# Performance work log

Hardware: AMD Instinct MI355X
Metric: run time of the kernel (lower is better)

## Reference

```python
import jax, jax.numpy as jnp
import numpy as np

H = 16  # head_count
NEG = -1e18

def setup_inputs() -> dict:
    key = jax.random.key(0)
    ks = jax.random.split(key, 8)
    B, L, D = 4, 2048, 1024
    s = 1.0 / np.sqrt(D)
    return {
        "key":   jax.random.normal(ks[0], (B, L, D), jnp.float32),
        "value": jax.random.normal(ks[1], (B, L, D), jnp.float32),
        "query": jax.random.normal(ks[2], (B, L, D), jnp.float32),
        "mask":  jax.random.randint(ks[3], (B, L, L), 0, 2).astype(bool),
        "Wk": jax.random.normal(ks[4], (D, D), jnp.float32) * s,
        "bk": jnp.zeros((D,), jnp.float32),
        "Wv": jax.random.normal(ks[5], (D, D), jnp.float32) * s,
        "bv": jnp.zeros((D,), jnp.float32),
        "Wq": jax.random.normal(ks[6], (D, D), jnp.float32) * s,
        "bq": jnp.zeros((D,), jnp.float32),
        "Wo": jax.random.normal(ks[7], (D, D), jnp.float32) * s,
        "bo": jnp.zeros((D,), jnp.float32),
    }

def reference(key, value, query, mask, Wk, bk, Wv, bv, Wq, bq, Wo, bo):
    B, Lk, D = key.shape
    Lq = query.shape[1]
    dh = D // H

    def shape(x, L):  # (B, L, D) -> (B, H, L, dh)
        return x.reshape(B, L, H, dh).transpose(0, 2, 1, 3)

    k = shape(key @ Wk + bk, Lk)
    v = shape(value @ Wv + bv, Lk)
    q = shape(query @ Wq + bq, Lq) / jnp.sqrt(jnp.asarray(dh, query.dtype))

    scores = jnp.einsum('bhqd,bhkd->bhqk', q, k).astype(jnp.float32)
    scores = jnp.where(mask[:, None, :, :], NEG, scores)  # masked_fill
    attn = jax.nn.softmax(scores, axis=-1).astype(q.dtype)
    # dropout is identity at inference
    ctx = jnp.einsum('bhqk,bhkd->bhqd', attn, v)
    ctx = ctx.transpose(0, 2, 1, 3).reshape(B, Lq, D)  # unshape
    output = ctx @ Wo + bo
    top_attn = attn[:, 0, :, :]
    return (output, top_attn)
```

## Files before the change

### kernel.cpp

```cpp
#include <hip/hip_runtime.h>
#include <hip/hip_bf16.h>
#include <stdint.h>

#define Bn 4
#define Ln 2048
#define Dn 1024
#define Hn 16
#define DHn 64

typedef __attribute__((ext_vector_type(8))) short short8;
typedef __attribute__((ext_vector_type(4))) float f32x4;
typedef unsigned long long u64;
typedef __hip_bfloat16 bf16;

union U8 { uint32_t u[4]; short8 s; };

__device__ __forceinline__ short f2b(float x) {
  bf16 b = __float2bfloat16(x);
  return *(short*)&b;
}

__device__ __forceinline__ uint32_t cvt_pk_bf16(float lo, float hi) {
  uint32_t r;
  asm("v_cvt_pk_bf16_f32 %0, %1, %2" : "=v"(r) : "v"(lo), "v"(hi));
  return r;
}

__device__ __forceinline__ void gll16(const void* g, void* l) {
  __builtin_amdgcn_global_load_lds(
      (const __attribute__((address_space(1))) void*)g,
      (__attribute__((address_space(3))) void*)l, 16, 0, 0);
}

__global__ __launch_bounds__(256) void f32_to_bf16_3(
    const float* __restrict__ A, const float* __restrict__ B2, const float* __restrict__ C3,
    short* __restrict__ oA, short* __restrict__ oB, short* __restrict__ oC, int n4)
{
  const int z = blockIdx.y;
  const float* in = (z == 0) ? A : (z == 1) ? B2 : C3;
  short* out = (z == 0) ? oA : (z == 1) ? oB : oC;
  int i = blockIdx.x * 256 + threadIdx.x;
  if (i < n4) {
    float4 v = ((const float4*)in)[i];
    short4 o;
    o.x = f2b(v.x); o.y = f2b(v.y); o.z = f2b(v.z); o.w = f2b(v.w);
    ((short4*)out)[i] = o;
  }
}

__global__ __launch_bounds__(256) void transpose_w_bf16(
    const float* __restrict__ W0, const float* __restrict__ W1,
    const float* __restrict__ W2, const float* __restrict__ W3,
    short* __restrict__ WT0, short* __restrict__ WT1,
    short* __restrict__ WT2, short* __restrict__ WT3)
{
  __shared__ float t[64][65];
  const int z = blockIdx.z;
  const float* src = (z == 0) ? W0 : (z == 1) ? W1 : (z == 2) ? W2 : W3;
  short* dst = (z == 0) ? WT0 : (z == 1) ? WT1 : (z == 2) ? WT2 : WT3;
  const int tid = threadIdx.x;
  const int k0 = blockIdx.x * 64, n0 = blockIdx.y * 64;
  #pragma unroll
  for (int it = 0; it < 4; ++it) {
    int idx = it * 256 + tid;
    int row = idx >> 4, c4 = (idx & 15) * 4;
    *(float4*)&t[row][c4] = *(const float4*)&src[(size_t)(k0 + row) * Dn + n0 + c4];
  }
  __syncthreads();
  #pragma unroll
  for (int it = 0; it < 4; ++it) {
    int idx = it * 256 + tid;
    int nr = idx >> 4, kc = (idx & 15) * 4;
    short4 o;
    o.x = f2b(t[kc + 0][nr]); o.y = f2b(t[kc + 1][nr]);
    o.z = f2b(t[kc + 2][nr]); o.w = f2b(t[kc + 3][nr]);
    *(short4*)&dst[(size_t)(n0 + nr) * Dn + k0 + kc] = o;
  }
}

__device__ __forceinline__ void gemm_core(
    const short* __restrict__ Xs, const short* __restrict__ WTs,
    const float* __restrict__ bias, void* __restrict__ Cout,
    int M, int N, int K, float scale, int mode)
{
  __shared__ short lds[2][2 * 128 * 32];
  const int tid  = threadIdx.x;
  const int lane = tid & 63;
  const int wv   = tid >> 6;
  const int quad = lane >> 4;
  const int l16  = lane & 15;
  const int m0 = blockIdx.y * 128, n0 = blockIdx.x * 128;
  const int wm = (wv >> 1) * 64, wn = (wv & 1) * 64;

  f32x4 acc[4][4];
  #pragma unroll
  for (int i = 0; i < 4; ++i)
    #pragma unroll
    for (int j = 0; j < 4; ++j)
      acc[i][j] = (f32x4){0.f, 0.f, 0.f, 0.f};

  #pragma unroll
  for (int r = 0; r < 2; ++r) {
    int idx = r * 256 + tid;
    int row = idx >> 2, kc = idx & 3;
    gll16(Xs  + (size_t)(m0 + row) * K + kc * 8, &lds[0][idx * 8]);
    gll16(WTs + (size_t)(n0 + row) * K + kc * 8, &lds[0][128 * 32 + idx * 8]);
  }
  __syncthreads();

  const int NT = K >> 5;
  int cur = 0;
  for (int t = 0; t < NT; ++t) {
    if (t + 1 < NT) {
      const int kn = (t + 1) * 32;
      #pragma unroll
      for (int r = 0; r < 2; ++r) {
        int idx = r * 256 + tid;
        int row = idx >> 2, kc = idx & 3;
        gll16(Xs  + (size_t)(m0 + row) * K + kn + kc * 8, &lds[cur ^ 1][idx * 8]);
        gll16(WTs + (size_t)(n0 + row) * K + kn + kc * 8, &lds[cur ^ 1][128 * 32 + idx * 8]);
      }
    }
    const short* ldsA = lds[cur];
    const short* ldsB = lds[cur] + 128 * 32;
    short8 af[4], bfr[4];
    #pragma unroll
    for (int i = 0; i < 4; ++i)
      af[i] = *(const short8*)(ldsA + (wm + i * 16 + l16) * 32 + quad * 8);
    #pragma unroll
    for (int j = 0; j < 4; ++j)
      bfr[j] = *(const short8*)(ldsB + (wn + j * 16 + l16) * 32 + quad * 8);
    __builtin_amdgcn_s_setprio(1);
    #pragma unroll
    for (int i = 0; i < 4; ++i)
      #pragma unroll
      for (int j = 0; j < 4; ++j)
        acc[i][j] = __builtin_amdgcn_mfma_f32_16x16x32_bf16(af[i], bfr[j], acc[i][j], 0, 0, 0);
    __builtin_amdgcn_s_setprio(0);
    __syncthreads();
    cur ^= 1;
  }

  if (mode == 0) {
    float* C = (float*)Cout;
    #pragma unroll
    for (int j = 0; j < 4; ++j) {
      int n = n0 + wn + j * 16 + l16;
      float bv = bias[n];
      #pragma unroll
      for (int i = 0; i < 4; ++i) {
        int mb = m0 + wm + i * 16 + quad * 4;
        #pragma unroll
        for (int r = 0; r < 4; ++r)
          C[(size_t)(mb + r) * N + n] = (acc[i][j][r] + bv) * scale;
      }
    }
  } else if (mode == 1) {
    short* C = (short*)Cout;
    #pragma unroll
    for (int j = 0; j < 4; ++j) {
      int n = n0 + wn + j * 16 + l16;
      float bv = bias[n];
      #pragma unroll
      for (int i = 0; i < 4; ++i) {
        int mb = m0 + wm + i * 16 + quad * 4;
        #pragma unroll
        for (int r = 0; r < 4; ++r)
          C[(size_t)(mb + r) * N + n] = f2b((acc[i][j][r] + bv) * scale);
      }
    }
  } else {
    short* C = (short*)Cout;
    #pragma unroll
    for (int j = 0; j < 4; ++j) {
      int n = n0 + wn + j * 16 + l16;
      float bv = bias[n];
      int hh = n >> 6, dd = n & 63;
      #pragma unroll
      for (int i = 0; i < 4; ++i) {
        int mb = m0 + wm + i * 16 + quad * 4;
        int bb = mb >> 11, ll = mb & 2047;
        short4 o;
        o.x = f2b((acc[i][j][0] + bv) * scale);
        o.y = f2b((acc[i][j][1] + bv) * scale);
        o.z = f2b((acc[i][j][2] + bv) * scale);
        o.w = f2b((acc[i][j][3] + bv) * scale);
        *(short4*)&C[((size_t)(bb * 16 + hh) * 64 + dd) * 2048 + ll] = o;
      }
    }
  }
}

__global__ __launch_bounds__(256) void gemm_qkv(
    const short* __restrict__ kc, const short* __restrict__ vc, const short* __restrict__ qc,
    const short* __restrict__ WkT, const short* __restrict__ WvT, const short* __restrict__ WqT,
    const float* __restrict__ bk, const float* __restrict__ bv, const float* __restrict__ bq,
    short* __restrict__ kb, short* __restrict__ vT, short* __restrict__ qb2)
{
  const int z = blockIdx.z;
  const short* Xs = (z == 0) ? kc : (z == 1) ? vc : qc;
  const short* WT = (z == 0) ? WkT : (z == 1) ? WvT : WqT;
  const float* bs = (z == 0) ? bk : (z == 1) ? bv : bq;
  void* C = (z == 0) ? (void*)kb : (z == 1) ? (void*)vT : (void*)qb2;
  float scale = (z == 2) ? 0.125f : 1.0f;
  int mode = (z == 1) ? 2 : 1;
  gemm_core(Xs, WT, bs, C, Bn * Ln, Dn, Dn, scale, mode);
}

__global__ __launch_bounds__(256) void gemm_wo(
    const short* __restrict__ ctx, const short* __restrict__ WoT,
    const float* __restrict__ bo, float* __restrict__ out)
{
  gemm_core(ctx, WoT, bo, out, Bn * Ln, Dn, Dn, 1.0f, 0);
}

__global__ __launch_bounds__(256) void pack_mask(const int* __restrict__ mask, u64* __restrict__ pm)
{
  size_t tg = (size_t)blockIdx.x * 256 + threadIdx.x;
  int v = mask[tg];
  u64 bal = __ballot(v != 0);
  if ((threadIdx.x & 63) == 0) pm[tg >> 6] = bal;
}


__device__ __forceinline__ const short8* ldsfrag(const short* lds, int row, int colb) {
  return (const short8*)((const char*)lds + row * 128 + (colb ^ ((row & 7) << 4)));
}

__global__ __launch_bounds__(256) void attn_fused(
    const short* __restrict__ qb, const short* __restrict__ kb,
    const short* __restrict__ vT, const u64* __restrict__ pm,
    short* __restrict__ ctx_bf, float* __restrict__ topattn,
    float* __restrict__ mtile, float2* __restrict__ stat2)
{
  __shared__ short ldsK[2][64 * 64];
  __shared__ short ldsVT[2][64 * 64];
  const int tid  = threadIdx.x;
  const int lane = tid & 63, wv = tid >> 6;
  const int quad = lane >> 4, l16 = lane & 15;
  const int g = blockIdx.x;
  const int x = (g >> 3) & 31;
  const int c = (g & 7) + ((g >> 8) << 3);
  const int h = c & 15, b = c >> 4;
  const int q0 = x * 64;
  const int q_g = q0 + wv * 16 + l16;

  const short* qrow = qb + (size_t)(b * Ln + q_g) * Dn + h * DHn;
  short8 qf[2];
  qf[0] = *(const short8*)(qrow + quad * 8);
  qf[1] = *(const short8*)(qrow + 32 + quad * 8);

  const u64* pmq = pm + (size_t)(b * Ln + q_g) * 32;
  const short* kbase = kb + (size_t)b * Ln * Dn + h * DHn;
  const short* vbase = vT + (size_t)(b * Hn + h) * DHn * Ln;

  #pragma unroll
  for (int it = 0; it < 2; ++it) {
    int idx = it * 256 + tid;
    int row = idx >> 3, cb = (idx & 7) * 16;
    int scb = cb ^ ((row & 7) << 4);
    gll16(kbase + (size_t)row * Dn + (scb >> 1), &ldsK[0][idx * 8]);
    gll16(vbase + (size_t)row * Ln + (scb >> 1), &ldsVT[0][idx * 8]);
  }
  __syncthreads();

  float m_r = -INFINITY, l_r = 0.f;
  f32x4 oc[4];
  #pragma unroll
  for (int dt = 0; dt < 4; ++dt) oc[dt] = (f32x4){0.f, 0.f, 0.f, 0.f};

  const int srcA = ((lane >> 4) & 1) * 32 + l16;
  const int srcB = srcA + 16;
  const bool hiHalf = (lane & 32) != 0;

  int cur = 0;
  for (int t = 0; t < 32; ++t) {
    const int k0 = t * 64;
    if (t < 31) {
      const int kn = k0 + 64;
      #pragma unroll
      for (int it = 0; it < 2; ++it) {
        int idx = it * 256 + tid;
        int row = idx >> 3, cb = (idx & 7) * 16;
        int scb = cb ^ ((row & 7) << 4);
        gll16(kbase + (size_t)(kn + row) * Dn + (scb >> 1), &ldsK[cur ^ 1][idx * 8]);
        gll16(vbase + (size_t)row * Ln + kn + (scb >> 1), &ldsVT[cur ^ 1][idx * 8]);
      }
    }

    f32x4 sv[4];
    #pragma unroll
    for (int mt = 0; mt < 4; ++mt) sv[mt] = (f32x4){0.f, 0.f, 0.f, 0.f};
    __builtin_amdgcn_s_setprio(1);
    #pragma unroll
    for (int s = 0; s < 2; ++s)
      #pragma unroll
      for (int mt = 0; mt < 4; ++mt) {
        short8 kf = *ldsfrag(&ldsK[cur][0], mt * 16 + l16, s * 64 + quad * 16);
        sv[mt] = __builtin_amdgcn_mfma_f32_16x16x32_bf16(kf, qf[s], sv[mt], 0, 0, 0);
      }
    __builtin_amdgcn_s_setprio(0);

    float tm = fmaxf(fmaxf(sv[0][0], sv[0][1]), fmaxf(sv[0][2], sv[0][3]));
    #pragma unroll
    for (int mt = 1; mt < 4; ++mt)
      tm = fmaxf(tm, fmaxf(fmaxf(sv[mt][0], sv[mt][1]), fmaxf(sv[mt][2], sv[mt][3])));
    tm = fmaxf(tm, __shfl_xor(tm, 16, 64));
    tm = fmaxf(tm, __shfl_xor(tm, 32, 64));
    if (tm > m_r + 8.f) {
      float sc = __expf(m_r - tm);
      l_r *= sc;
      #pragma unroll
      for (int dt = 0; dt < 4; ++dt)
        #pragma unroll
        for (int r = 0; r < 4; ++r) oc[dt][r] *= sc;
      m_r = tm;
    }
    const u64 w = pmq[t];
    float ls = 0.f;
    #pragma unroll
    for (int mt = 0; mt < 4; ++mt) {
      unsigned nib = (unsigned)(w >> (mt * 16 + quad * 4)) & 0xFu;
      #pragma unroll
      for (int r = 0; r < 4; ++r) {
        float p = __expf(sv[mt][r] - m_r);
        p = (nib & (1u << r)) ? 0.f : p;
        sv[mt][r] = p;
        ls += p;
      }
    }
    l_r += ls;

    if (h == 0) {
      float* tpb = topattn + (size_t)(b * Ln + q_g) * Ln + k0 + quad * 4;
      #pragma unroll
      for (int mt = 0; mt < 4; ++mt)
        *(float4*)&tpb[mt * 16] = *(float4*)&sv[mt];
      if (quad == 0) mtile[(size_t)(b * Ln + q_g) * 32 + t] = m_r;
    }

    uint32_t d0[4], d1[4];
    #pragma unroll
    for (int mt = 0; mt < 4; ++mt) {
      d0[mt] = cvt_pk_bf16(sv[mt][0], sv[mt][1]);
      d1[mt] = cvt_pk_bf16(sv[mt][2], sv[mt][3]);
    }

    #pragma unroll
    for (int ks = 0; ks < 2; ++ks) {
      uint32_t a0  = (uint32_t)__shfl((int)d0[2 * ks],     srcA, 64);
      uint32_t a0b = (uint32_t)__shfl((int)d0[2 * ks + 1], srcA, 64);
      uint32_t a1  = (uint32_t)__shfl((int)d1[2 * ks],     srcA, 64);
      uint32_t a1b = (uint32_t)__shfl((int)d1[2 * ks + 1], srcA, 64);
      uint32_t b0  = (uint32_t)__shfl((int)d0[2 * ks],     srcB, 64);
      uint32_t b0b = (uint32_t)__shfl((int)d0[2 * ks + 1], srcB, 64);
      uint32_t b1  = (uint32_t)__shfl((int)d1[2 * ks],     srcB, 64);
      uint32_t b1b = (uint32_t)__shfl((int)d1[2 * ks + 1], srcB, 64);
      U8 u;
      u.u[0] = hiHalf ? a0b : a0;
      u.u[1] = hiHalf ? a1b : a1;
      u.u[2] = hiHalf ? b0b : b0;
      u.u[3] = hiHalf ? b1b : b1;
      short8 pf = u.s;
      __builtin_amdgcn_s_setprio(1);
      #pragma unroll
      for (int dt = 0; dt < 4; ++dt) {
        short8 vf = *ldsfrag(&ldsVT[cur][0], dt * 16 + l16, ks * 64 + quad * 16);
        oc[dt] = __builtin_amdgcn_mfma_f32_16x16x32_bf16(vf, pf, oc[dt], 0, 0, 0);
      }
      __builtin_amdgcn_s_setprio(0);
    }
    __syncthreads();
    cur ^= 1;
  }

  l_r += __shfl_xor(l_r, 16, 64);
  l_r += __shfl_xor(l_r, 32, 64);
  const float rinv = (l_r > 0.f) ? 1.f / l_r : 0.f;

  short* crow = ctx_bf + (size_t)(b * Ln + q_g) * Dn + h * DHn;
  #pragma unroll
  for (int dt = 0; dt < 4; ++dt) {
    short4 o;
    o.x = f2b(oc[dt][0] * rinv); o.y = f2b(oc[dt][1] * rinv);
    o.z = f2b(oc[dt][2] * rinv); o.w = f2b(oc[dt][3] * rinv);
    *(short4*)&crow[dt * 16 + quad * 4] = o;
  }
  if (h == 0 && quad == 0)
    stat2[b * Ln + q_g] = make_float2(m_r, rinv);
}

__global__ __launch_bounds__(256) void topattn_fix(
    float* __restrict__ topattn, const float* __restrict__ mtile,
    const float2* __restrict__ stat2)
{
  const int row = blockIdx.x;
  const float2 st = stat2[row];
  const int tid = threadIdx.x;
  const float sc = __expf(mtile[(size_t)row * 32 + (tid >> 3)] - st.x) * st.y;
  float4* p = (float4*)(topattn + (size_t)row * Ln) + tid * 2;
  float4 a = p[0], b2 = p[1];
  a.x *= sc; a.y *= sc; a.z *= sc; a.w *= sc;
  b2.x *= sc; b2.y *= sc; b2.z *= sc; b2.w *= sc;
  p[0] = a; p[1] = b2;
}

extern "C" void kernel_launch(void* const* d_in, const int* in_sizes, int n_in,
                              void* d_out, int out_size, void* d_ws, size_t ws_size,
                              hipStream_t stream) {
  (void)in_sizes; (void)n_in; (void)out_size; (void)ws_size;
  const float* key   = (const float*)d_in[0];
  const float* value = (const float*)d_in[1];
  const float* query = (const float*)d_in[2];
  const int*   mask  = (const int*)d_in[3];
  const float* Wk = (const float*)d_in[4];
  const float* bk = (const float*)d_in[5];
  const float* Wv = (const float*)d_in[6];
  const float* bv = (const float*)d_in[7];
  const float* Wq = (const float*)d_in[8];
  const float* bq = (const float*)d_in[9];
  const float* Wo = (const float*)d_in[10];
  const float* bo = (const float*)d_in[11];

  char* ws = (char*)d_ws;
  const size_t MiB = 1ull << 20;
  short* kc  = (short*)(ws +   0 * MiB);
  short* vc  = (short*)(ws +  16 * MiB);
  short* qc  = (short*)(ws +  32 * MiB);
  short* WkT = (short*)(ws +  48 * MiB);
  short* WvT = (short*)(ws +  50 * MiB);
  short* WqT = (short*)(ws +  52 * MiB);
  short* WoT = (short*)(ws +  54 * MiB);
  short* qb  = (short*)(ws +  56 * MiB);
  short* kb  = (short*)(ws +  72 * MiB);
  short* vT  = (short*)(ws +  88 * MiB);
  u64*   pm  = (u64*)  (ws + 104 * MiB);
  short* ctx_bf = (short*)(ws + 106 * MiB);
  float* mtile  = (float*)(ws + 122 * MiB);
  float2* stat2 = (float2*)(ws + 123 * MiB);

  float* out     = (float*)d_out;
  float* topattn = out + (size_t)Bn * Ln * Dn;

  const int M = Bn * Ln;
  const int n4 = (M * Dn) / 4;

  f32_to_bf16_3<<<dim3(n4 / 256, 3), 256, 0, stream>>>(key, value, query, kc, vc, qc, n4);
  transpose_w_bf16<<<dim3(16, 16, 4), 256, 0, stream>>>(Wk, Wv, Wq, Wo, WkT, WvT, WqT, WoT);

  gemm_qkv<<<dim3(8, 64, 3), 256, 0, stream>>>(kc, vc, qc, WkT, WvT, WqT, bk, bv, bq, kb, vT, qb);

  pack_mask<<<dim3((Bn * Ln * Ln) / 256), 256, 0, stream>>>(mask, pm);

  attn_fused<<<dim3(2048), 256, 0, stream>>>(qb, kb, vT, pm, ctx_bf, topattn, mtile, stat2);
  topattn_fix<<<dim3(Bn * Ln), 256, 0, stream>>>(topattn, mtile, stat2);

  gemm_wo<<<dim3(8, 64), 256, 0, stream>>>(ctx_bf, WoT, bo, out);
}
```

Measured before the change: 564.7 us.

## Use 128-query tiles with 8 waves and exchange P through LDS

The attention kernel now runs 512 threads per block, with 8 waves covering 128 query rows. Each K/V tile loaded into LDS is therefore shared by twice as many queries, and each thread issues one async load per buffer instead of two. The cross-lane shuffle that rearranged the softmax probabilities into the MFMA B-operand layout is replaced by a write to a per-wave LDS scratch array followed by a vector read. The cost is fewer blocks in the grid, more LDS per block, and extra LDS traffic for P.

```diff
diff --git a/kernel.cpp b/kernel.cpp
--- a/kernel.cpp
+++ b/kernel.cpp
@@ -9,11 +9,10 @@
 #define DHn 64
 
 typedef __attribute__((ext_vector_type(8))) short short8;
+typedef __attribute__((ext_vector_type(4))) short short4v;
 typedef __attribute__((ext_vector_type(4))) float f32x4;
 typedef unsigned long long u64;
 typedef __hip_bfloat16 bf16;
-
-union U8 { uint32_t u[4]; short8 s; };
 
 __device__ __forceinline__ short f2b(float x) {
   bf16 b = __float2bfloat16(x);
@@ -227,7 +226,7 @@
   return (const short8*)((const char*)lds + row * 128 + (colb ^ ((row & 7) << 4)));
 }
 
-__global__ __launch_bounds__(256) void attn_fused(
+__global__ __launch_bounds__(512) void attn_fused(
     const short* __restrict__ qb, const short* __restrict__ kb,
     const short* __restrict__ vT, const u64* __restrict__ pm,
     short* __restrict__ ctx_bf, float* __restrict__ topattn,
@@ -235,14 +234,15 @@
 {
   __shared__ short ldsK[2][64 * 64];
   __shared__ short ldsVT[2][64 * 64];
+  __shared__ short pp[8][16][72];
   const int tid  = threadIdx.x;
   const int lane = tid & 63, wv = tid >> 6;
   const int quad = lane >> 4, l16 = lane & 15;
   const int g = blockIdx.x;
-  const int x = (g >> 3) & 31;
-  const int c = (g & 7) + ((g >> 8) << 3);
+  const int x = (g >> 3) & 15;
+  const int c = ((g >> 7) << 3) | (g & 7);
   const int h = c & 15, b = c >> 4;
-  const int q0 = x * 64;
+  const int q0 = x * 128;
   const int q_g = q0 + wv * 16 + l16;
 
   const short* qrow = qb + (size_t)(b * Ln + q_g) * Dn + h * DHn;
@@ -254,38 +254,24 @@
   const short* kbase = kb + (size_t)b * Ln * Dn + h * DHn;
   const short* vbase = vT + (size_t)(b * Hn + h) * DHn * Ln;
 
-  #pragma unroll
-  for (int it = 0; it < 2; ++it) {
-    int idx = it * 256 + tid;
-    int row = idx >> 3, cb = (idx & 7) * 16;
-    int scb = cb ^ ((row & 7) << 4);
-    gll16(kbase + (size_t)row * Dn + (scb >> 1), &ldsK[0][idx * 8]);
-    gll16(vbase + (size_t)row * Ln + (scb >> 1), &ldsVT[0][idx * 8]);
-  }
+  const int srow = tid >> 3, scb = ((tid & 7) * 16) ^ ((srow & 7) << 4);
+
+  gll16(kbase + (size_t)srow * Dn + (scb >> 1), &ldsK[0][tid * 8]);
+  gll16(vbase + (size_t)srow * Ln + (scb >> 1), &ldsVT[0][tid * 8]);
   __syncthreads();
 
   float m_r = -INFINITY, l_r = 0.f;
   f32x4 oc[4];
   #pragma unroll
   for (int dt = 0; dt < 4; ++dt) oc[dt] = (f32x4){0.f, 0.f, 0.f, 0.f};
-
-  const int srcA = ((lane >> 4) & 1) * 32 + l16;
-  const int srcB = srcA + 16;
-  const bool hiHalf = (lane & 32) != 0;
 
   int cur = 0;
   for (int t = 0; t < 32; ++t) {
     const int k0 = t * 64;
     if (t < 31) {
       const int kn = k0 + 64;
-      #pragma unroll
-      for (int it = 0; it < 2; ++it) {
-        int idx = it * 256 + tid;
-        int row = idx >> 3, cb = (idx & 7) * 16;
-        int scb = cb ^ ((row & 7) << 4);
-        gll16(kbase + (size_t)(kn + row) * Dn + (scb >> 1), &ldsK[cur ^ 1][idx * 8]);
-        gll16(vbase + (size_t)row * Ln + kn + (scb >> 1), &ldsVT[cur ^ 1][idx * 8]);
-      }
+      gll16(kbase + (size_t)(kn + srow) * Dn + (scb >> 1), &ldsK[cur ^ 1][tid * 8]);
+      gll16(vbase + (size_t)srow * Ln + kn + (scb >> 1), &ldsVT[cur ^ 1][tid * 8]);
     }
 
     f32x4 sv[4];
@@ -339,29 +325,17 @@
       if (quad == 0) mtile[(size_t)(b * Ln + q_g) * 32 + t] = m_r;
     }
 
-    uint32_t d0[4], d1[4];
     #pragma unroll
     for (int mt = 0; mt < 4; ++mt) {
-      d0[mt] = cvt_pk_bf16(sv[mt][0], sv[mt][1]);
-      d1[mt] = cvt_pk_bf16(sv[mt][2], sv[mt][3]);
+      union { uint32_t u[2]; short4v s4; } pu;
+      pu.u[0] = cvt_pk_bf16(sv[mt][0], sv[mt][1]);
+      pu.u[1] = cvt_pk_bf16(sv[mt][2], sv[mt][3]);
+      *(short4v*)&pp[wv][l16][mt * 16 + quad * 4] = pu.s4;
     }
 
     #pragma unroll
     for (int ks = 0; ks < 2; ++ks) {
-      uint32_t a0  = (uint32_t)__shfl((int)d0[2 * ks],     srcA, 64);
-      uint32_t a0b = (uint32_t)__shfl((int)d0[2 * ks + 1], srcA, 64);
-      uint32_t a1  = (uint32_t)__shfl((int)d1[2 * ks],     srcA, 64);
-      uint32_t a1b = (uint32_t)__shfl((int)d1[2 * ks + 1], srcA, 64);
-      uint32_t b0  = (uint32_t)__shfl((int)d0[2 * ks],     srcB, 64);
-      uint32_t b0b = (uint32_t)__shfl((int)d0[2 * ks + 1], srcB, 64);
-      uint32_t b1  = (uint32_t)__shfl((int)d1[2 * ks],     srcB, 64);
-      uint32_t b1b = (uint32_t)__shfl((int)d1[2 * ks + 1], srcB, 64);
-      U8 u;
-      u.u[0] = hiHalf ? a0b : a0;
-      u.u[1] = hiHalf ? a1b : a1;
-      u.u[2] = hiHalf ? b0b : b0;
-      u.u[3] = hiHalf ? b1b : b1;
-      short8 pf = u.s;
+      short8 pf = *(const short8*)&pp[wv][l16][ks * 32 + quad * 8];
       __builtin_amdgcn_s_setprio(1);
       #pragma unroll
       for (int dt = 0; dt < 4; ++dt) {
@@ -452,7 +426,7 @@
 
   pack_mask<<<dim3((Bn * Ln * Ln) / 256), 256, 0, stream>>>(mask, pm);
 
-  attn_fused<<<dim3(2048), 256, 0, stream>>>(qb, kb, vT, pm, ctx_bf, topattn, mtile, stat2);
+  attn_fused<<<dim3(1024), 512, 0, stream>>>(qb, kb, vT, pm, ctx_bf, topattn, mtile, stat2);
   topattn_fix<<<dim3(Bn * Ln), 256, 0, stream>>>(topattn, mtile, stat2);
 
   gemm_wo<<<dim3(8, 64), 256, 0, stream>>>(ctx_bf, WoT, bo, out);
```

New measurement: 543.1 us. -3.8%, faster.
